# Kernel tuning notes

Hardware: AMD Instinct MI355X
Metric: run time of the kernel (lower is better)

The kernel has to match this reference:

```python
import math
import jax, jax.numpy as jnp
import numpy as np

K_NEIGH = 8  # module's self.k

def setup_inputs() -> dict:
    key = jax.random.key(0)
    ks = jax.random.split(key, 5)
    B, N, D = 4, 4096, 256
    s = 1.0 / math.sqrt(D)
    return {
        "x": jax.random.normal(ks[0], (B, N, D), dtype=jnp.float32),
        "Wqkv": jax.random.normal(ks[1], (3 * D, D), dtype=jnp.float32) * s,
        "bqkv": jax.random.normal(ks[2], (3 * D,), dtype=jnp.float32) * 0.02,
        "Wout": jax.random.normal(ks[3], (D, D), dtype=jnp.float32) * s,
        "bout": jax.random.normal(ks[4], (D,), dtype=jnp.float32) * 0.02,
    }

def reference(x, Wqkv, bqkv, Wout, bout):
    B, N, D = x.shape
    qkv = x @ Wqkv.T + bqkv                      # [B,N,3D]
    q, k, v = jnp.split(qkv, 3, axis=-1)         # each [B,N,D]
    # F.normalize(k, dim=-1) with eps=1e-12
    kn = k / jnp.maximum(jnp.linalg.norm(k, axis=-1, keepdims=True), 1e-12)
    sim = jnp.einsum('bnd,bmd->bnm', kn, kn)     # [B,N,N] cosine similarity
    sim = sim - 1e9 * jnp.eye(N, dtype=sim.dtype)
    k_val = min(K_NEIGH, N - 1)
    _, idx = jax.lax.top_k(sim, k_val)           # [B,N,k] neighbor indices
    # NOTE: the torch code builds k.unsqueeze(2).expand(B,N,N,D) and gathers on
    # dim 2, but that tensor is CONSTANT along dim 2, so the gather reduces to a
    # broadcast of k (and v) over the neighbor axis -- reproduced faithfully:
    k_sel = jnp.broadcast_to(k[:, :, None, :], (B, N, k_val, D))
    v_sel = jnp.broadcast_to(v[:, :, None, :], (B, N, k_val, D))
    scores = jnp.sum(q[:, :, None, :] * k_sel, axis=-1) / math.sqrt(D)  # [B,N,k]
    attn = jax.nn.softmax(scores, axis=-1)
    out = jnp.sum(attn[..., None] * v_sel, axis=2)                      # [B,N,D]
    return x + out @ Wout.T + bout
```

## Files before the change

### kernel.cpp

```cpp
#include <hip/hip_runtime.h>
#include <hip/hip_bf16.h>

#define DD 256
#define NROWS 16384
#define TILES 4
#define TROWS 16

typedef float f32x4 __attribute__((ext_vector_type(4)));
typedef __bf16 bf16x4 __attribute__((ext_vector_type(4)));
typedef __bf16 bf16x8 __attribute__((ext_vector_type(8)));

__device__ __forceinline__ void gl2lds16(const void* g, void* l) {
  __builtin_amdgcn_global_load_lds(
      (const __attribute__((address_space(1))) void*)g,
      (__attribute__((address_space(3))) void*)l, 16, 0, 0);
}

__device__ __forceinline__ bf16x8 cvt8(f32x4 lo, f32x4 hi) {
  bf16x8 v;
#pragma unroll
  for (int j = 0; j < 4; ++j) {
    v[j] = (__bf16)lo[j];
    v[4 + j] = (__bf16)hi[j];
  }
  return v;
}

__global__ __launch_bounds__(256) void wc_bc_kernel(
    const float* __restrict__ Wqkv, const float* __restrict__ bqkv,
    const float* __restrict__ Wout, const float* __restrict__ bout,
    __bf16* __restrict__ Wc, float* __restrict__ bc) {
  __shared__ f32x4 part[4][64];
  __shared__ float red[4];
  const int i = blockIdx.x;
  const int t = threadIdx.x;
  const int w = t >> 6, l = t & 63;
  const float* __restrict__ Wv = Wqkv + 2 * DD * DD;
  const float* __restrict__ bv = bqkv + 2 * DD;
  const float* __restrict__ wrow = Wout + (size_t)i * DD;

  f32x4 wr[16];
#pragma unroll
  for (int k = 0; k < 16; ++k) wr[k] = *(const f32x4*)(wrow + w * 64 + k * 4);

  const float* wvp = Wv + (size_t)(w * 64) * DD + l * 4;
  f32x4 a0 = {0.f, 0.f, 0.f, 0.f}, a1 = {0.f, 0.f, 0.f, 0.f};
  f32x4 a2 = {0.f, 0.f, 0.f, 0.f}, a3 = {0.f, 0.f, 0.f, 0.f};
#pragma unroll
  for (int k = 0; k < 16; ++k) {
    a0 += wr[k][0] * *(const f32x4*)(wvp + (size_t)(4 * k + 0) * DD);
    a1 += wr[k][1] * *(const f32x4*)(wvp + (size_t)(4 * k + 1) * DD);
    a2 += wr[k][2] * *(const f32x4*)(wvp + (size_t)(4 * k + 2) * DD);
    a3 += wr[k][3] * *(const f32x4*)(wvp + (size_t)(4 * k + 3) * DD);
  }
  part[w][l] = (a0 + a1) + (a2 + a3);

  {
    const int d = w * 64 + l;
    float p = wrow[d] * bv[d];
#pragma unroll
    for (int off = 32; off > 0; off >>= 1) p += __shfl_down(p, off);
    if (l == 0) red[w] = p;
  }
  __syncthreads();
  if (w == 0) {
    f32x4 s = (part[0][l] + part[1][l]) + (part[2][l] + part[3][l]);
    bf16x4 o;
#pragma unroll
    for (int j = 0; j < 4; ++j) o[j] = (__bf16)s[j];
    *(bf16x4*)(Wc + (size_t)i * DD + l * 4) = o;
    if (l == 0) bc[i] = bout[i] + red[0] + red[1] + red[2] + red[3];
  }
}

__global__ __launch_bounds__(256, 3) void knn_attn_main(
    const float* __restrict__ x, const __bf16* __restrict__ Wc,
    const float* __restrict__ bc, float* __restrict__ out) {
  __shared__ __bf16 wc_s[64 * DD];
  __shared__ __bf16 xs[2][TROWS * DD];

  const int t = threadIdx.x;
  const int w = t >> 6, l = t & 63;
  const int cg = blockIdx.x >> 8;
  const int rb = blockIdx.x & 255;
  const int C0 = cg * 64;
  const int Rbase = rb * (TILES * TROWS);

#pragma unroll
  for (int j = 0; j < 8; ++j) {
    const int L = (w * 8 + j) * 1024 + l * 16;
    const int row = L >> 9;
    const int srow = (L & 511) ^ ((row & 7) << 4);
    gl2lds16((const char*)Wc + (size_t)(C0 + row) * 512 + srow,
             (char*)wc_s + (w * 8192 + j * 1024));
  }

  const int sr = t >> 4, sc = t & 15;
  const int ssw = (sr & 7) << 4;
  const int sbase = sr * 512 + sc * 32;

  const int xrow = l & 15, g4 = l >> 4;
  const int rsw = (xrow & 7) << 4;
  const int rA = w * 16 + xrow;
  const int csw = (rA & 7) << 4;
  const int ocol = C0 + w * 16 + g4 * 4;
  const f32x4 bias = *(const f32x4*)(bc + ocol);

  {
    const float* s0 = x + (size_t)(Rbase + sr) * DD + sc * 16;
    f32x4 a = *(const f32x4*)(s0 + 0);
    f32x4 b = *(const f32x4*)(s0 + 4);
    f32x4 c = *(const f32x4*)(s0 + 8);
    f32x4 d = *(const f32x4*)(s0 + 12);
    char* xb = (char*)&xs[0][0];
    *(bf16x8*)(xb + ((sbase + 0) ^ ssw)) = cvt8(a, b);
    *(bf16x8*)(xb + ((sbase + 16) ^ ssw)) = cvt8(c, d);
  }
  __syncthreads();

  for (int i = 0; i < TILES; ++i) {
    f32x4 a, b, c, d;
    if (i + 1 < TILES) {
      const float* sn = x + (size_t)(Rbase + (i + 1) * TROWS + sr) * DD + sc * 16;
      a = *(const f32x4*)(sn + 0);
      b = *(const f32x4*)(sn + 4);
      c = *(const f32x4*)(sn + 8);
      d = *(const f32x4*)(sn + 12);
    }

    const char* xb = (const char*)&xs[i & 1][0];
    f32x4 acc = {0.f, 0.f, 0.f, 0.f};
#pragma unroll
    for (int ks = 0; ks < 8; ++ks) {
      const int kb = ks * 64 + g4 * 16;
      bf16x8 bfr = *(const bf16x8*)(xb + ((xrow * 512 + kb) ^ rsw));
      bf16x8 af = *(const bf16x8*)((const char*)wc_s + ((rA * 512 + kb) ^ csw));
      acc = __builtin_amdgcn_mfma_f32_16x16x32_bf16(af, bfr, acc, 0, 0, 0);
    }
    {
      const size_t idx = (size_t)(Rbase + i * TROWS + xrow) * DD + ocol;
      f32x4 xres = *(const f32x4*)(x + idx);
      *(f32x4*)(out + idx) = acc + xres + bias;
    }

    if (i + 1 < TILES) {
      char* xbn = (char*)&xs[(i + 1) & 1][0];
      *(bf16x8*)(xbn + ((sbase + 0) ^ ssw)) = cvt8(a, b);
      *(bf16x8*)(xbn + ((sbase + 16) ^ ssw)) = cvt8(c, d);
    }
    __syncthreads();
  }
}

extern "C" void kernel_launch(void* const* d_in, const int* in_sizes, int n_in,
                              void* d_out, int out_size, void* d_ws, size_t ws_size,
                              hipStream_t stream) {
  const float* x = (const float*)d_in[0];
  const float* Wqkv = (const float*)d_in[1];
  const float* bqkv = (const float*)d_in[2];
  const float* Wout = (const float*)d_in[3];
  const float* bout = (const float*)d_in[4];
  float* out = (float*)d_out;

  __bf16* Wc = (__bf16*)d_ws;
  float* bc = (float*)((char*)d_ws + DD * DD * sizeof(__bf16));

  wc_bc_kernel<<<DD, 256, 0, stream>>>(Wqkv, bqkv, Wout, bout, Wc, bc);
  knn_attn_main<<<1024, 256, 0, stream>>>(x, Wc, bc, out);
}
```

Measured before the change: 22.82 us.

## Hold weight fragments in registers and widen the weight-combine kernel

```diff
diff --git a/kernel.cpp b/kernel.cpp
--- a/kernel.cpp
+++ b/kernel.cpp
@@ -10,12 +10,6 @@
 typedef __bf16 bf16x4 __attribute__((ext_vector_type(4)));
 typedef __bf16 bf16x8 __attribute__((ext_vector_type(8)));
 
-__device__ __forceinline__ void gl2lds16(const void* g, void* l) {
-  __builtin_amdgcn_global_load_lds(
-      (const __attribute__((address_space(1))) void*)g,
-      (__attribute__((address_space(3))) void*)l, 16, 0, 0);
-}
-
 __device__ __forceinline__ bf16x8 cvt8(f32x4 lo, f32x4 hi) {
   bf16x8 v;
 #pragma unroll
@@ -26,11 +20,11 @@
   return v;
 }
 
-__global__ __launch_bounds__(256) void wc_bc_kernel(
+__global__ __launch_bounds__(1024) void wc_bc_kernel(
     const float* __restrict__ Wqkv, const float* __restrict__ bqkv,
     const float* __restrict__ Wout, const float* __restrict__ bout,
     __bf16* __restrict__ Wc, float* __restrict__ bc) {
-  __shared__ f32x4 part[4][64];
+  __shared__ f32x4 part[16][64];
   __shared__ float red[4];
   const int i = blockIdx.x;
   const int t = threadIdx.x;
@@ -39,15 +33,15 @@
   const float* __restrict__ bv = bqkv + 2 * DD;
   const float* __restrict__ wrow = Wout + (size_t)i * DD;
 
-  f32x4 wr[16];
+  f32x4 wr[4];
 #pragma unroll
-  for (int k = 0; k < 16; ++k) wr[k] = *(const f32x4*)(wrow + w * 64 + k * 4);
+  for (int k = 0; k < 4; ++k) wr[k] = *(const f32x4*)(wrow + w * 16 + k * 4);
 
-  const float* wvp = Wv + (size_t)(w * 64) * DD + l * 4;
+  const float* wvp = Wv + (size_t)(w * 16) * DD + l * 4;
   f32x4 a0 = {0.f, 0.f, 0.f, 0.f}, a1 = {0.f, 0.f, 0.f, 0.f};
   f32x4 a2 = {0.f, 0.f, 0.f, 0.f}, a3 = {0.f, 0.f, 0.f, 0.f};
 #pragma unroll
-  for (int k = 0; k < 16; ++k) {
+  for (int k = 0; k < 4; ++k) {
     a0 += wr[k][0] * *(const f32x4*)(wvp + (size_t)(4 * k + 0) * DD);
     a1 += wr[k][1] * *(const f32x4*)(wvp + (size_t)(4 * k + 1) * DD);
     a2 += wr[k][2] * *(const f32x4*)(wvp + (size_t)(4 * k + 2) * DD);
@@ -55,16 +49,17 @@
   }
   part[w][l] = (a0 + a1) + (a2 + a3);
 
-  {
-    const int d = w * 64 + l;
-    float p = wrow[d] * bv[d];
+  if (t < 256) {
+    float p = wrow[t] * bv[t];
 #pragma unroll
     for (int off = 32; off > 0; off >>= 1) p += __shfl_down(p, off);
     if (l == 0) red[w] = p;
   }
   __syncthreads();
   if (w == 0) {
-    f32x4 s = (part[0][l] + part[1][l]) + (part[2][l] + part[3][l]);
+    f32x4 s = {0.f, 0.f, 0.f, 0.f};
+#pragma unroll
+    for (int k = 0; k < 16; ++k) s += part[k][l];
     bf16x4 o;
 #pragma unroll
     for (int j = 0; j < 4; ++j) o[j] = (__bf16)s[j];
@@ -73,10 +68,9 @@
   }
 }
 
-__global__ __launch_bounds__(256, 3) void knn_attn_main(
+__global__ __launch_bounds__(256, 4) void knn_attn_main(
     const float* __restrict__ x, const __bf16* __restrict__ Wc,
     const float* __restrict__ bc, float* __restrict__ out) {
-  __shared__ __bf16 wc_s[64 * DD];
   __shared__ __bf16 xs[2][TROWS * DD];
 
   const int t = threadIdx.x;
@@ -86,25 +80,22 @@
   const int C0 = cg * 64;
   const int Rbase = rb * (TILES * TROWS);
 
+  const int xrow = l & 15, g4 = l >> 4;
+  const int rsw = (xrow & 7) << 4;
+  const int rA = w * 16 + xrow;
+  const int ocol = C0 + w * 16 + g4 * 4;
+
+  bf16x8 af[8];
+  {
+    const __bf16* wrp = Wc + (size_t)(C0 + rA) * DD + g4 * 8;
 #pragma unroll
-  for (int j = 0; j < 8; ++j) {
-    const int L = (w * 8 + j) * 1024 + l * 16;
-    const int row = L >> 9;
-    const int srow = (L & 511) ^ ((row & 7) << 4);
-    gl2lds16((const char*)Wc + (size_t)(C0 + row) * 512 + srow,
-             (char*)wc_s + (w * 8192 + j * 1024));
+    for (int ks = 0; ks < 8; ++ks) af[ks] = *(const bf16x8*)(wrp + ks * 32);
   }
+  const f32x4 bias = *(const f32x4*)(bc + ocol);
 
   const int sr = t >> 4, sc = t & 15;
   const int ssw = (sr & 7) << 4;
   const int sbase = sr * 512 + sc * 32;
-
-  const int xrow = l & 15, g4 = l >> 4;
-  const int rsw = (xrow & 7) << 4;
-  const int rA = w * 16 + xrow;
-  const int csw = (rA & 7) << 4;
-  const int ocol = C0 + w * 16 + g4 * 4;
-  const f32x4 bias = *(const f32x4*)(bc + ocol);
 
   {
     const float* s0 = x + (size_t)(Rbase + sr) * DD + sc * 16;
@@ -121,7 +112,8 @@
   for (int i = 0; i < TILES; ++i) {
     f32x4 a, b, c, d;
     if (i + 1 < TILES) {
-      const float* sn = x + (size_t)(Rbase + (i + 1) * TROWS + sr) * DD + sc * 16;
+      const float* sn =
+          x + (size_t)(Rbase + (i + 1) * TROWS + sr) * DD + sc * 16;
       a = *(const f32x4*)(sn + 0);
       b = *(const f32x4*)(sn + 4);
       c = *(const f32x4*)(sn + 8);
@@ -134,8 +126,7 @@
     for (int ks = 0; ks < 8; ++ks) {
       const int kb = ks * 64 + g4 * 16;
       bf16x8 bfr = *(const bf16x8*)(xb + ((xrow * 512 + kb) ^ rsw));
-      bf16x8 af = *(const bf16x8*)((const char*)wc_s + ((rA * 512 + kb) ^ csw));
-      acc = __builtin_amdgcn_mfma_f32_16x16x32_bf16(af, bfr, acc, 0, 0, 0);
+      acc = __builtin_amdgcn_mfma_f32_16x16x32_bf16(af[ks], bfr, acc, 0, 0, 0);
     }
     {
       const size_t idx = (size_t)(Rbase + i * TROWS + xrow) * DD + ocol;
@@ -165,6 +156,6 @@
   __bf16* Wc = (__bf16*)d_ws;
   float* bc = (float*)((char*)d_ws + DD * DD * sizeof(__bf16));
 
-  wc_bc_kernel<<<DD, 256, 0, stream>>>(Wqkv, bqkv, Wout, bout, Wc, bc);
+  wc_bc_kernel<<<DD, 1024, 0, stream>>>(Wqkv, bqkv, Wout, bout, Wc, bc);
   knn_attn_main<<<1024, 256, 0, stream>>>(x, Wc, bc, out);
 }
```

Result: no change. 23.14 us (+1.4%).
